# Kernel optimization log

Measured on AMD Instinct MI355X. Metric: run time of the kernel, lower is better.

The kernel has to match this reference:

```python
import jax, jax.numpy as jnp
import numpy as np

B, L, D = 16, 1024, 1024
OUT_LEN = 24
N_LAYERS = 3
CYCLE = L
LN_EPS = 1e-5


def _make_pe(seq_len, hidden, cycle):
    # pe[t, j] = 2*pi*t/cycle, then sin on even cols, cos on odd cols
    t = jnp.arange(seq_len, dtype=jnp.float32)[:, None]
    base = (2.0 * jnp.pi * t / cycle) * jnp.ones((1, hidden), jnp.float32)
    cols = jnp.arange(hidden)
    return jnp.where((cols % 2 == 0)[None, :], jnp.sin(base), jnp.cos(base))


def setup_inputs() -> dict:
    key = jax.random.key(0)
    ks = jax.random.split(key, 12)
    s = 0.02
    return {
        "x": jax.random.normal(ks[0], (B, L, D), jnp.float32),
        "pe": _make_pe(L, D, CYCLE),
        "w1": jax.random.normal(ks[1], (N_LAYERS, D, D), jnp.float32) * s,
        "b1": jnp.zeros((N_LAYERS, D), jnp.float32),
        "w2": jax.random.normal(ks[2], (N_LAYERS, D, D), jnp.float32) * s,
        "b2": jnp.zeros((N_LAYERS, D), jnp.float32),
        "ln_g": jnp.ones((N_LAYERS, D), jnp.float32),
        "ln_b": jnp.zeros((N_LAYERS, D), jnp.float32),
        "fc_w": jax.random.normal(ks[3], (1, D), jnp.float32) * s,
        "fc_b": jnp.zeros((1,), jnp.float32),
        "final_w": jax.random.normal(ks[4], (OUT_LEN, L), jnp.float32) * s,
        "final_b": jnp.zeros((OUT_LEN,), jnp.float32),
    }


def _layer_norm(y, g, b):
    mu = jnp.mean(y, axis=-1, keepdims=True)
    var = jnp.mean((y - mu) ** 2, axis=-1, keepdims=True)
    return (y - mu) * jax.lax.rsqrt(var + LN_EPS) * g + b


def reference(x, pe, w1, b1, w2, b2, ln_g, ln_b, fc_w, fc_b, final_w, final_b):
    d = x.shape[-1]
    scale = 1.0 / jnp.sqrt(jnp.float32(d))
    # positional add (pe[:, :seq_len]; here L == D so this is the full buffer)
    h = x + pe[:, : x.shape[1]]
    attns = []
    for l in range(w1.shape[0]):
        # hand-rolled bmm-softmax-bmm self-attention (q = k = v = h)
        scores = jnp.einsum("bqd,bkd->bqk", h, h) * scale  # (B, L, L)
        a = jax.nn.softmax(scores, axis=-1)
        ctx = jnp.einsum("bqk,bkd->bqd", a, h)
        # position-wise FFN with hidden == D, residual over ctx, then LN
        ff = jnp.maximum(ctx @ w1[l].T + b1[l], 0.0) @ w2[l].T + b2[l]
        h = _layer_norm(ctx + ff, ln_g[l], ln_b[l])
        attns.append(a)
    # final head: D -> 1, squeeze, then L -> OUT_LEN over the sequence dim
    z = (h @ fc_w.T + fc_b)[..., 0]  # (B, L)
    out = z @ final_w.T + final_b    # (B, OUT_LEN)
    return (out, jnp.stack(attns))
```

## Files before the change

kernel.cpp:

```cpp
#include <hip/hip_runtime.h>

typedef unsigned short u16;
typedef __attribute__((ext_vector_type(8))) short short8;
typedef __attribute__((ext_vector_type(4))) float f32x4;
typedef __attribute__((ext_vector_type(4))) unsigned short u16x4;

__device__ __forceinline__ float bf2f(u16 u){
  union { unsigned int i; float f; } x; x.i = ((unsigned int)u) << 16; return x.f;
}
__device__ __forceinline__ u16 f2bf(float f){
  union { float f; unsigned int i; } x; x.f = f;
  return (u16)((x.i + 0x7fffu + ((x.i >> 16) & 1u)) >> 16);
}
__device__ __forceinline__ void async16(const void* g, void* s){
  __builtin_amdgcn_global_load_lds((const __attribute__((address_space(1))) void*)g,
                                   (__attribute__((address_space(3))) void*)s, 16, 0, 0);
}

__global__ __launch_bounds__(256) void k_split2(const float* __restrict__ s1, u16* __restrict__ d1,
                                                const float* __restrict__ s2, u16* __restrict__ d2){
  long i = ((long)blockIdx.x * 256 + threadIdx.x) * 4;
  f32x4 v1 = *(const f32x4*)(s1 + i);
  f32x4 v2 = *(const f32x4*)(s2 + i);
  u16x4 h1, h2;
  #pragma unroll
  for (int j=0;j<4;j++){ h1[j] = f2bf(v1[j]); h2[j] = f2bf(v2[j]); }
  *(u16x4*)(d1+i) = h1;
  *(u16x4*)(d2+i) = h2;
}

__global__ __launch_bounds__(256) void k_addpe(const float* __restrict__ x, const float* __restrict__ pe,
                                               u16* __restrict__ d){
  long i = ((long)blockIdx.x * 256 + threadIdx.x) * 4;
  f32x4 xv = *(const f32x4*)(x + i);
  f32x4 pv = *(const f32x4*)(pe + (i & 1048575));
  u16x4 hh;
  #pragma unroll
  for (int j=0;j<4;j++) hh[j] = f2bf(xv[j]+pv[j]);
  *(u16x4*)(d+i) = hh;
}

__global__ __launch_bounds__(256) void k_transpose(const u16* __restrict__ in, u16* __restrict__ outp){
  __shared__ u16 tile[64][68];
  const long b = blockIdx.z;
  const int d0 = blockIdx.x * 64, l0 = blockIdx.y * 64;
  const long ibase = b * 1048576l;
  const int t = threadIdx.x;
  const int cr = t >> 4;
  const int cc = (t & 15) * 4;
  #pragma unroll
  for (int rr=0; rr<4; rr++){
    int row = cr + rr*16;
    u16x4 v = *(const u16x4*)(in + ibase + (long)(l0+row)*1024 + d0 + cc);
    *(u16x4*)&tile[row][cc] = v;
  }
  __syncthreads();
  #pragma unroll
  for (int rr=0; rr<4; rr++){
    int drow = cr + rr*16;
    u16x4 y;
    y[0] = tile[cc+0][drow];
    y[1] = tile[cc+1][drow];
    y[2] = tile[cc+2][drow];
    y[3] = tile[cc+3][drow];
    *(u16x4*)(outp + ibase + (long)(d0+drow)*1024 + l0 + cc) = y;
  }
}

__global__ __launch_bounds__(512, 1) void attn_sm(
    const u16* __restrict__ hB, float* __restrict__ probs, u16* __restrict__ pB)
{
  __shared__ __align__(16) u16 sm[65536];
  const int t = threadIdx.x;
  const int w = t >> 6, lane = t & 63;
  const int fr = lane & 15, fs = lane >> 4;

  const int p = blockIdx.x;
  const int id = (p & 7) * 32 + (p >> 3);
  const long bz = id >> 4;
  const int brow = (id & 15) << 6;

  const u16* hb = hB + bz * 1048576l;

  const u16* gsrc[8];
  int gdst[8];
  #pragma unroll
  for (int c=0;c<8;c++){
    int u = c*512 + t;
    int row = u >> 2;
    int slot = (u & 3) ^ ((row >> 1) & 3);
    gsrc[c] = hb + (long)row*1024 + slot*8;
    gdst[c] = c*4096 + w*512;
  }

  int offA[4], offB[8];
  #pragma unroll
  for (int i=0;i<4;i++){
    int x = i*16 + fr;
    offA[i] = (brow + x)*32 + (fs ^ (((brow + x)>>1)&3))*8;
  }
  #pragma unroll
  for (int j=0;j<8;j++){
    int x = w*128 + j*16 + fr;
    offB[j] = x*32 + (fs ^ ((x>>1)&3))*8;
  }

  f32x4 acc[4][8];
  #pragma unroll
  for (int i=0;i<4;i++)
    #pragma unroll
    for (int j=0;j<8;j++) acc[i][j] = (f32x4){0.f,0.f,0.f,0.f};

  #pragma unroll
  for (int c=0;c<8;c++) async16(gsrc[c], sm + gdst[c]);
  asm volatile("s_waitcnt vmcnt(0)" ::: "memory");
  __builtin_amdgcn_s_barrier();
  __builtin_amdgcn_sched_barrier(0);

#define ATT_BODY(BUF)                                                          \
    short8 aF[4], bF[8];                                                       \
    _Pragma("unroll")                                                          \
    for (int i=0;i<4;i++) aF[i] = *(const short8*)((BUF) + offA[i]);           \
    _Pragma("unroll")                                                          \
    for (int j=0;j<8;j++) bF[j] = *(const short8*)((BUF) + offB[j]);           \
    __builtin_amdgcn_s_setprio(1);                                             \
    _Pragma("unroll")                                                          \
    for (int i=0;i<4;i++)                                                      \
      _Pragma("unroll")                                                        \
      for (int j=0;j<8;j++)                                                    \
        acc[i][j] = __builtin_amdgcn_mfma_f32_16x16x32_bf16(aF[i], bF[j], acc[i][j], 0,0,0); \
    __builtin_amdgcn_s_setprio(0);

  for (int kt = 0; kt < 31; ++kt){
    const u16* buf = sm + (kt & 1)*32768;
    u16* stg = sm + ((kt + 1) & 1)*32768;
    const int ko = (kt + 1)*32;
    #pragma unroll
    for (int c=0;c<8;c++) async16(gsrc[c] + ko, stg + gdst[c]);
    ATT_BODY(buf)
    asm volatile("s_waitcnt vmcnt(0)" ::: "memory");
    __builtin_amdgcn_s_barrier();
    __builtin_amdgcn_sched_barrier(0);
  }
  {
    const u16* buf = sm + 32768;
    ATT_BODY(buf)
  }
#undef ATT_BODY

  float* red = (float*)sm;
  const float SC = 0.03125f;

  float mx[4][4];
  #pragma unroll
  for (int i=0;i<4;i++)
    #pragma unroll
    for (int q=0;q<4;q++){
      float m = acc[i][0][q];
      #pragma unroll
      for (int j=1;j<8;j++) m = fmaxf(m, acc[i][j][q]);
      #pragma unroll
      for (int d=1; d<16; d<<=1) m = fmaxf(m, __shfl_xor(m, d));
      mx[i][q] = m;
    }
  if (fr == 0){
    #pragma unroll
    for (int i=0;i<4;i++)
      #pragma unroll
      for (int q=0;q<4;q++) red[(i*16 + fs*4 + q)*8 + w] = mx[i][q];
  }
  __syncthreads();
  float M[4][4];
  #pragma unroll
  for (int i=0;i<4;i++)
    #pragma unroll
    for (int q=0;q<4;q++){
      const int row = i*16 + fs*4 + q;
      f32x4 a = *(const f32x4*)&red[row*8];
      f32x4 b = *(const f32x4*)&red[row*8+4];
      M[i][q] = fmaxf(fmaxf(fmaxf(a[0],a[1]),fmaxf(a[2],a[3])),
                      fmaxf(fmaxf(b[0],b[1]),fmaxf(b[2],b[3])));
    }
  float sum[4][4];
  #pragma unroll
  for (int i=0;i<4;i++)
    #pragma unroll
    for (int q=0;q<4;q++){
      float s = 0.f;
      #pragma unroll
      for (int j=0;j<8;j++){
        float e = expf((acc[i][j][q] - M[i][q]) * SC);
        acc[i][j][q] = e;
        s += e;
      }
      #pragma unroll
      for (int d=1; d<16; d<<=1) s += __shfl_xor(s, d);
      sum[i][q] = s;
    }
  __syncthreads();
  if (fr == 0){
    #pragma unroll
    for (int i=0;i<4;i++)
      #pragma unroll
      for (int q=0;q<4;q++) red[(i*16 + fs*4 + q)*8 + w] = sum[i][q];
  }
  __syncthreads();
  float inv[4][4];
  #pragma unroll
  for (int i=0;i<4;i++)
    #pragma unroll
    for (int q=0;q<4;q++){
      const int row = i*16 + fs*4 + q;
      f32x4 a = *(const f32x4*)&red[row*8];
      f32x4 b = *(const f32x4*)&red[row*8+4];
      inv[i][q] = 1.0f / (a[0]+a[1]+a[2]+a[3]+b[0]+b[1]+b[2]+b[3]);
    }

  const long obase = bz * 1048576l;
  #pragma unroll
  for (int i=0;i<4;i++)
    #pragma unroll
    for (int q=0;q<4;q++){
      const long rbase = obase + (long)(brow + i*16 + fs*4 + q)*1024;
      const float iv = inv[i][q];
      #pragma unroll
      for (int j=0;j<8;j++){
        const int col = w*128 + j*16 + fr;
        const float pv = acc[i][j][q] * iv;
        probs[rbase + col] = pv;
        pB[rbase + col] = f2bf(pv);
      }
    }
}

template<int MODE>
__global__ __launch_bounds__(512, 2) void gemm8(
    const u16* __restrict__ aB, const u16* __restrict__ bB,
    int per, long sA, long sB, long sC,
    int lda, int ldb, int ldc,
    float scale, const float* __restrict__ bias,
    const u16* __restrict__ res,
    float* __restrict__ cF, u16* __restrict__ cB)
{
  __shared__ __align__(16) u16 sm[65536];
  const int t = threadIdx.x;
  const int w = t >> 6, lane = t & 63;
  const int wm = w >> 2, wn = w & 3;
  const int fr = lane & 15, fs = lane >> 4;

  const int p = blockIdx.x;
  const int chunk = gridDim.x >> 3;
  const int id = (p & 7) * chunk + (p >> 3);
  const long bz = id / per;
  const int rem = id % per;
  const int m0 = (rem >> 2) << 8, n0 = (rem & 3) << 8;

  const u16* a = aB + bz * sA;
  const u16* b = bB + bz * sB;

  const int urow = t >> 2;
  const int col8 = ((t & 3) ^ ((t >> 3) & 3)) * 8;
  const u16* gA0 = a + (long)(m0 + urow) * lda + col8;
  const u16* gA1 = a + (long)(m0 + 128 + urow) * lda + col8;
  const u16* gB0 = b + (long)(n0 + urow) * ldb + col8;
  const u16* gB1 = b + (long)(n0 + 128 + urow) * ldb + col8;
  u16* dA0 = sm + (w << 9);
  u16* dA1 = sm + 4096 + (w << 9);
  u16* dB0 = sm + 8192 + (w << 9);
  u16* dB1 = sm + 12288 + (w << 9);

  int offA[8], offB[4];
  #pragma unroll
  for (int i=0;i<8;i++){
    int row = wm*128 + i*16 + fr;
    int sl = fs ^ ((row >> 1) & 3);
    offA[i] = row*32 + sl*8;
  }
  #pragma unroll
  for (int j=0;j<4;j++){
    int row = wn*64 + j*16 + fr;
    int sl = fs ^ ((row >> 1) & 3);
    offB[j] = 8192 + row*32 + sl*8;
  }

  f32x4 acc[8][4];
  #pragma unroll
  for (int i=0;i<8;i++)
    #pragma unroll
    for (int j=0;j<4;j++) acc[i][j] = (f32x4){0.f,0.f,0.f,0.f};

  #pragma unroll
  for (int pb=0; pb<3; ++pb){
    const int kb = pb*32, sb = pb*16384;
    async16(gA0+kb, dA0+sb); async16(gA1+kb, dA1+sb);
    async16(gB0+kb, dB0+sb); async16(gB1+kb, dB1+sb);
  }
  gA0 += 96; gA1 += 96; gB0 += 96; gB1 += 96;
  asm volatile("s_waitcnt vmcnt(8)" ::: "memory");
  __builtin_amdgcn_s_barrier();
  __builtin_amdgcn_sched_barrier(0);

#define KT_PHASE(SMB, I0, I1, STG, RDB)                                        \
  { short8 a0 = *(const short8*)((SMB) + offA[I0]);                            \
    short8 a1 = *(const short8*)((SMB) + offA[I1]);                            \
    RDB                                                                        \
    STG                                                                        \
    __builtin_amdgcn_sched_barrier(0);                                         \
    __builtin_amdgcn_s_barrier();                                              \
    __builtin_amdgcn_sched_barrier(0);                                         \
    __builtin_amdgcn_s_setprio(1);                                             \
    acc[I0][0] = __builtin_amdgcn_mfma_f32_16x16x32_bf16(a0, bF[0], acc[I0][0], 0,0,0); \
    acc[I0][1] = __builtin_amdgcn_mfma_f32_16x16x32_bf16(a0, bF[1], acc[I0][1], 0,0,0); \
    acc[I0][2] = __builtin_amdgcn_mfma_f32_16x16x32_bf16(a0, bF[2], acc[I0][2], 0,0,0); \
    acc[I0][3] = __builtin_amdgcn_mfma_f32_16x16x32_bf16(a0, bF[3], acc[I0][3], 0,0,0); \
    acc[I1][0] = __builtin_amdgcn_mfma_f32_16x16x32_bf16(a1, bF[0], acc[I1][0], 0,0,0); \
    acc[I1][1] = __builtin_amdgcn_mfma_f32_16x16x32_bf16(a1, bF[1], acc[I1][1], 0,0,0); \
    acc[I1][2] = __builtin_amdgcn_mfma_f32_16x16x32_bf16(a1, bF[2], acc[I1][2], 0,0,0); \
    acc[I1][3] = __builtin_amdgcn_mfma_f32_16x16x32_bf16(a1, bF[3], acc[I1][3], 0,0,0); \
    __builtin_amdgcn_s_setprio(0);                                             \
  }

#define KT_BODY4(SMB, ST0, ST1, ST2, ST3)                                      \
  { short8 bF[4];                                                              \
    KT_PHASE(SMB, 0, 1, ST0,                                                   \
      { bF[0] = *(const short8*)((SMB) + offB[0]);                             \
        bF[1] = *(const short8*)((SMB) + offB[1]);                             \
        bF[2] = *(const short8*)((SMB) + offB[2]);                             \
        bF[3] = *(const short8*)((SMB) + offB[3]); })                          \
    KT_PHASE(SMB, 2, 3, ST1, {})                                               \
    KT_PHASE(SMB, 4, 5, ST2, {})                                               \
    KT_PHASE(SMB, 6, 7, ST3, {})                                               \
  }

  for (int kt = 0; kt < 29; ++kt){
    const u16* smb = sm + (kt & 3)*16384;
    const int sb = ((kt + 3) & 3)*16384;
    KT_BODY4(smb,
      { async16(gA0, dA0+sb); gA0 += 32; },
      { async16(gA1, dA1+sb); gA1 += 32; },
      { async16(gB0, dB0+sb); gB0 += 32; },
      { async16(gB1, dB1+sb); gB1 += 32; })
    asm volatile("s_waitcnt vmcnt(8)" ::: "memory");
    __builtin_amdgcn_s_barrier();
    __builtin_amdgcn_sched_barrier(0);
  }
  {
    const u16* smb = sm + (29 & 3)*16384;
    KT_BODY4(smb, {}, {}, {}, {})
    asm volatile("s_waitcnt vmcnt(4)" ::: "memory");
    __builtin_amdgcn_s_barrier();
    __builtin_amdgcn_sched_barrier(0);
  }
  {
    const u16* smb = sm + (30 & 3)*16384;
    KT_BODY4(smb, {}, {}, {}, {})
    asm volatile("s_waitcnt vmcnt(0)" ::: "memory");
    __builtin_amdgcn_s_barrier();
    __builtin_amdgcn_sched_barrier(0);
  }
  {
    const u16* smb = sm + (31 & 3)*16384;
    KT_BODY4(smb, {}, {}, {}, {})
  }
#undef KT_BODY4
#undef KT_PHASE

  const long cBase = bz * sC;
  const int rb = m0 + wm*128 + fs*4;
  const int cb = n0 + wn*64 + fr;
  #pragma unroll
  for (int j=0;j<4;j++){
    const int c = cb + j*16;
    float bv = 0.f;
    if constexpr (MODE == 2 || MODE == 3) bv = bias[c];
    #pragma unroll
    for (int i=0;i<8;i++){
      #pragma unroll
      for (int q=0;q<4;q++){
        const int r = rb + i*16 + q;
        const long idx = cBase + (long)r*ldc + c;
        float v = acc[i][j][q];
        if constexpr (MODE == 1){
          cB[idx] = f2bf(v);
        } else if constexpr (MODE == 2){
          cB[idx] = f2bf(fmaxf(v + bv, 0.f));
        } else {
          cF[idx] = v + bv + bf2f(res[idx]);
        }
      }
    }
  }
}

__global__ __launch_bounds__(256) void k_ln(const float* __restrict__ r,
                                            const float* __restrict__ g, const float* __restrict__ b,
                                            u16* __restrict__ h){
  const long row = blockIdx.x;
  const float* rr = r + row * 1024;
  const int t = threadIdx.x, w = t >> 6, lane = t & 63;
  __shared__ float rA[4], rB[4];
  f32x4 v = *(const f32x4*)(rr + t*4);
  float s = v[0]+v[1]+v[2]+v[3];
  #pragma unroll
  for (int off=32; off; off>>=1) s += __shfl_xor(s, off);
  if (lane==0) rA[w] = s;
  __syncthreads();
  const float mu = (rA[0]+rA[1]+rA[2]+rA[3]) * (1.0f/1024.0f);
  float sq = 0.f;
  #pragma unroll
  for (int j=0;j<4;j++){ float d = v[j]-mu; sq += d*d; }
  #pragma unroll
  for (int off=32; off; off>>=1) sq += __shfl_xor(sq, off);
  if (lane==0) rB[w] = sq;
  __syncthreads();
  const float var = (rB[0]+rB[1]+rB[2]+rB[3]) * (1.0f/1024.0f);
  const float inv = rsqrtf(var + 1e-5f);
  u16x4 hh;
  #pragma unroll
  for (int j=0;j<4;j++){
    int d = t*4+j;
    hh[j] = f2bf((v[j]-mu)*inv*g[d] + b[d]);
  }
  *(u16x4*)(h + row*1024 + t*4) = hh;
}

__global__ __launch_bounds__(256) void k_final1(const u16* __restrict__ h,
                                                const float* __restrict__ fw, const float* __restrict__ fb,
                                                float* __restrict__ z){
  const int row = blockIdx.x*4 + (threadIdx.x>>6);
  const int lane = threadIdx.x & 63;
  const long base = (long)row * 1024;
  const int d0 = lane * 16;
  float s = 0.f;
  #pragma unroll
  for (int j=0;j<16;j++){
    int d = d0 + j;
    s += bf2f(h[base+d]) * fw[d];
  }
  #pragma unroll
  for (int off=32; off; off>>=1) s += __shfl_xor(s, off);
  if (lane==0) z[row] = s + fb[0];
}

__global__ __launch_bounds__(256) void k_final2(const float* __restrict__ z,
                                                const float* __restrict__ fw, const float* __restrict__ fb,
                                                float* __restrict__ out){
  const int idx = blockIdx.x*4 + (threadIdx.x>>6);
  const int lane = threadIdx.x & 63;
  const int b = idx / 24, o = idx % 24;
  float s = 0.f;
  #pragma unroll
  for (int j=0;j<16;j++){
    int li = lane + j*64;
    s += z[b*1024 + li] * fw[o*1024 + li];
  }
  #pragma unroll
  for (int off=32; off; off>>=1) s += __shfl_xor(s, off);
  if (lane==0) out[idx] = s + fb[o];
}

extern "C" void kernel_launch(void* const* d_in, const int* in_sizes, int n_in,
                              void* d_out, int out_size, void* d_ws, size_t ws_size,
                              hipStream_t stream){
  const float* x   = (const float*)d_in[0];
  const float* pe  = (const float*)d_in[1];
  const float* w1  = (const float*)d_in[2];
  const float* b1  = (const float*)d_in[3];
  const float* w2  = (const float*)d_in[4];
  const float* b2  = (const float*)d_in[5];
  const float* lng = (const float*)d_in[6];
  const float* lnb = (const float*)d_in[7];
  const float* fcw = (const float*)d_in[8];
  const float* fcb = (const float*)d_in[9];
  const float* fw  = (const float*)d_in[10];
  const float* fb  = (const float*)d_in[11];
  float* out  = (float*)d_out;
  float* attn = out + 384;

  char* ws = (char*)d_ws;
  const long BB = 32l*1024*1024;
  u16* hB = (u16*)(ws + 0*BB);
  u16* tB = (u16*)(ws + 1*BB);
  u16* cB = (u16*)(ws + 2*BB);
  u16* pB = (u16*)(ws + 3*BB);
  float* rf = (float*)(ws + 4*BB);
  u16* w1B = (u16*)(ws + 6*BB);
  u16* w2B = w1B + 3l*1024*1024;
  float* z = (float*)(w2B + 3l*1024*1024);

  const long M1 = 1024l*1024;

  k_split2<<<3072, 256, 0, stream>>>(w1, w1B, w2, w2B);
  k_addpe<<<16384, 256, 0, stream>>>(x, pe, hB);
  k_transpose<<<dim3(16,16,16), 256, 0, stream>>>(hB, tB);

  for (int l = 0; l < 3; l++){
    float* sc = attn + (long)l*16*M1;
    attn_sm<<<256, 512, 0, stream>>>(hB, sc, pB);
    gemm8<1><<<256, 512, 0, stream>>>(pB, tB, 16, M1,M1,M1, 1024,1024,1024,
        1.f, nullptr, nullptr, nullptr, cB);
    gemm8<2><<<256, 512, 0, stream>>>(cB, w1B+l*M1, 256, 0,0,0, 1024,1024,1024,
        1.f, b1+l*1024, nullptr, nullptr, pB);
    gemm8<3><<<256, 512, 0, stream>>>(pB, w2B+l*M1, 256, 0,0,0, 1024,1024,1024,
        1.f, b2+l*1024, cB, rf, nullptr);
    k_ln<<<16384, 256, 0, stream>>>(rf, lng+l*1024, lnb+l*1024, hB);
    if (l < 2) k_transpose<<<dim3(16,16,16), 256, 0, stream>>>(hB, tB);
  }

  k_final1<<<4096, 256, 0, stream>>>(hB, fcw, fcb, z);
  k_final2<<<96, 256, 0, stream>>>(z, fw, fb, out);
}
```

Measured before the change: 726.3 us.

## Stage attention K tiles via registers and store pre-LN residual in bf16

The attention kernel's main loop now prefetches the next K tile into registers with ordinary global loads and writes it to LDS after the MFMA body, replacing the async global-to-LDS copies. The FFN output plus residual is written as bf16 instead of fp32, and layer norm reads bf16, halving that round-trip traffic. The gemm strides and scale arguments are hardcoded to 1024 and removed. The bf16 residual adds rounding before layer norm, and register staging raises register pressure in a kernel already holding a 4x8 accumulator array.

```diff
diff --git a/kernel.cpp b/kernel.cpp
--- a/kernel.cpp
+++ b/kernel.cpp
@@ -83,15 +83,14 @@
   const u16* hb = hB + bz * 1048576l;
 
   const u16* gsrc[8];
-  int gdst[8];
   #pragma unroll
   for (int c=0;c<8;c++){
     int u = c*512 + t;
     int row = u >> 2;
     int slot = (u & 3) ^ ((row >> 1) & 3);
     gsrc[c] = hb + (long)row*1024 + slot*8;
-    gdst[c] = c*4096 + w*512;
-  }
+  }
+  const int gdst0 = t*8;
 
   int offA[4], offB[8];
   #pragma unroll
@@ -112,7 +111,7 @@
     for (int j=0;j<8;j++) acc[i][j] = (f32x4){0.f,0.f,0.f,0.f};
 
   #pragma unroll
-  for (int c=0;c<8;c++) async16(gsrc[c], sm + gdst[c]);
+  for (int c=0;c<8;c++) async16(gsrc[c], sm + c*4096 + (w<<9));
   asm volatile("s_waitcnt vmcnt(0)" ::: "memory");
   __builtin_amdgcn_s_barrier();
   __builtin_amdgcn_sched_barrier(0);
@@ -133,12 +132,15 @@
 
   for (int kt = 0; kt < 31; ++kt){
     const u16* buf = sm + (kt & 1)*32768;
-    u16* stg = sm + ((kt + 1) & 1)*32768;
+    u16* wb = sm + ((kt + 1) & 1)*32768 + gdst0;
     const int ko = (kt + 1)*32;
-    #pragma unroll
-    for (int c=0;c<8;c++) async16(gsrc[c] + ko, stg + gdst[c]);
+    short8 pf[8];
+    #pragma unroll
+    for (int c=0;c<8;c++) pf[c] = *(const short8*)(gsrc[c] + ko);
     ATT_BODY(buf)
-    asm volatile("s_waitcnt vmcnt(0)" ::: "memory");
+    #pragma unroll
+    for (int c=0;c<8;c++) *(short8*)(wb + c*4096) = pf[c];
+    asm volatile("s_waitcnt lgkmcnt(0)" ::: "memory");
     __builtin_amdgcn_s_barrier();
     __builtin_amdgcn_sched_barrier(0);
   }
@@ -237,10 +239,8 @@
 __global__ __launch_bounds__(512, 2) void gemm8(
     const u16* __restrict__ aB, const u16* __restrict__ bB,
     int per, long sA, long sB, long sC,
-    int lda, int ldb, int ldc,
-    float scale, const float* __restrict__ bias,
-    const u16* __restrict__ res,
-    float* __restrict__ cF, u16* __restrict__ cB)
+    const float* __restrict__ bias, const u16* __restrict__ res,
+    u16* __restrict__ cB)
 {
   __shared__ __align__(16) u16 sm[65536];
   const int t = threadIdx.x;
@@ -260,10 +260,10 @@
 
   const int urow = t >> 2;
   const int col8 = ((t & 3) ^ ((t >> 3) & 3)) * 8;
-  const u16* gA0 = a + (long)(m0 + urow) * lda + col8;
-  const u16* gA1 = a + (long)(m0 + 128 + urow) * lda + col8;
-  const u16* gB0 = b + (long)(n0 + urow) * ldb + col8;
-  const u16* gB1 = b + (long)(n0 + 128 + urow) * ldb + col8;
+  const u16* gA0 = a + (long)(m0 + urow) * 1024 + col8;
+  const u16* gA1 = a + (long)(m0 + 128 + urow) * 1024 + col8;
+  const u16* gB0 = b + (long)(n0 + urow) * 1024 + col8;
+  const u16* gB1 = b + (long)(n0 + 128 + urow) * 1024 + col8;
   u16* dA0 = sm + (w << 9);
   u16* dA1 = sm + 4096 + (w << 9);
   u16* dB0 = sm + 8192 + (w << 9);
@@ -378,28 +378,31 @@
       #pragma unroll
       for (int q=0;q<4;q++){
         const int r = rb + i*16 + q;
-        const long idx = cBase + (long)r*ldc + c;
+        const long idx = cBase + (long)r*1024 + c;
         float v = acc[i][j][q];
         if constexpr (MODE == 1){
           cB[idx] = f2bf(v);
         } else if constexpr (MODE == 2){
           cB[idx] = f2bf(fmaxf(v + bv, 0.f));
         } else {
-          cF[idx] = v + bv + bf2f(res[idx]);
+          cB[idx] = f2bf(v + bv + bf2f(res[idx]));
         }
       }
     }
   }
 }
 
-__global__ __launch_bounds__(256) void k_ln(const float* __restrict__ r,
+__global__ __launch_bounds__(256) void k_ln(const u16* __restrict__ r,
                                             const float* __restrict__ g, const float* __restrict__ b,
                                             u16* __restrict__ h){
   const long row = blockIdx.x;
-  const float* rr = r + row * 1024;
+  const u16* rr = r + row * 1024;
   const int t = threadIdx.x, w = t >> 6, lane = t & 63;
   __shared__ float rA[4], rB[4];
-  f32x4 v = *(const f32x4*)(rr + t*4);
+  u16x4 rv = *(const u16x4*)(rr + t*4);
+  f32x4 v;
+  #pragma unroll
+  for (int j=0;j<4;j++) v[j] = bf2f(rv[j]);
   float s = v[0]+v[1]+v[2]+v[3];
   #pragma unroll
   for (int off=32; off; off>>=1) s += __shfl_xor(s, off);
@@ -483,7 +486,7 @@
   u16* tB = (u16*)(ws + 1*BB);
   u16* cB = (u16*)(ws + 2*BB);
   u16* pB = (u16*)(ws + 3*BB);
-  float* rf = (float*)(ws + 4*BB);
+  u16* rfB = (u16*)(ws + 4*BB);
   u16* w1B = (u16*)(ws + 6*BB);
   u16* w2B = w1B + 3l*1024*1024;
   float* z = (float*)(w2B + 3l*1024*1024);
@@ -497,13 +500,13 @@
   for (int l = 0; l < 3; l++){
     float* sc = attn + (long)l*16*M1;
     attn_sm<<<256, 512, 0, stream>>>(hB, sc, pB);
-    gemm8<1><<<256, 512, 0, stream>>>(pB, tB, 16, M1,M1,M1, 1024,1024,1024,
-        1.f, nullptr, nullptr, nullptr, cB);
-    gemm8<2><<<256, 512, 0, stream>>>(cB, w1B+l*M1, 256, 0,0,0, 1024,1024,1024,
-        1.f, b1+l*1024, nullptr, nullptr, pB);
-    gemm8<3><<<256, 512, 0, stream>>>(pB, w2B+l*M1, 256, 0,0,0, 1024,1024,1024,
-        1.f, b2+l*1024, cB, rf, nullptr);
-    k_ln<<<16384, 256, 0, stream>>>(rf, lng+l*1024, lnb+l*1024, hB);
+    gemm8<1><<<256, 512, 0, stream>>>(pB, tB, 16, M1,M1,M1,
+        nullptr, nullptr, cB);
+    gemm8<2><<<256, 512, 0, stream>>>(cB, w1B+l*M1, 256, 0,0,0,
+        b1+l*1024, nullptr, pB);
+    gemm8<3><<<256, 512, 0, stream>>>(pB, w2B+l*M1, 256, 0,0,0,
+        b2+l*1024, cB, rfB);
+    k_ln<<<16384, 256, 0, stream>>>(rfB, lng+l*1024, lnb+l*1024, hB);
     if (l < 2) k_transpose<<<dim3(16,16,16), 256, 0, stream>>>(hB, tB);
   }
 
```

Result: slower. 788.7 us (+8.6%).
